# Kernel tuning notes

Hardware: AMD Instinct MI355X
Metric: run time of the kernel (lower is better)

Reference implementation:

```python
import jax, jax.numpy as jnp
import numpy as np

N_NODES = 50000
N_EDGES = 800000
NEG_SLOPE = 0.2


def _gat_layer(x, src, dst, W, al, ar, n_nodes):
    """Single multi-head GAT conv (DGL-style). Returns [N, H, D]."""
    H, D = al.shape
    feat = (x @ W).reshape(n_nodes, H, D)              # [N,H,D]
    el = jnp.einsum('nhd,hd->nh', feat, al)            # [N,H]
    er = jnp.einsum('nhd,hd->nh', feat, ar)            # [N,H]
    e = jax.nn.leaky_relu(el[src] + er[dst], NEG_SLOPE)  # [E,H]
    # numerically-stable edge softmax over incoming edges per dst node
    emax = jax.ops.segment_max(e, dst, num_segments=n_nodes)  # [N,H]
    emax = jnp.where(jnp.isfinite(emax), emax, 0.0)
    ee = jnp.exp(e - emax[dst])                        # [E,H]
    denom = jax.ops.segment_sum(ee, dst, num_segments=n_nodes)  # [N,H]
    alpha = ee / (denom[dst] + 1e-9)                   # [E,H]
    msg = alpha[:, :, None] * feat[src]                # [E,H,D]
    return jax.ops.segment_sum(msg, dst, num_segments=n_nodes)  # [N,H,D]


def setup_inputs() -> dict:
    key = jax.random.key(0)
    ks = jax.random.split(key, 9)
    features = jax.random.normal(ks[0], (N_NODES, 512), jnp.float32)
    src = jax.random.randint(ks[1], (N_EDGES,), 0, N_NODES)
    dst = jax.random.randint(ks[2], (N_EDGES,), 0, N_NODES)
    W1 = jax.random.normal(ks[3], (512, 256), jnp.float32) * 0.05
    al1 = jax.random.normal(ks[4], (8, 32), jnp.float32) * 0.05
    ar1 = jax.random.normal(ks[5], (8, 32), jnp.float32) * 0.05
    W2 = jax.random.normal(ks[6], (256, 320), jnp.float32) * 0.05
    al2 = jax.random.normal(ks[7], (8, 40), jnp.float32) * 0.05
    ar2 = jax.random.normal(ks[8], (8, 40), jnp.float32) * 0.05
    return {"features": features, "src": src, "dst": dst,
            "W1": W1, "al1": al1, "ar1": ar1,
            "W2": W2, "al2": al2, "ar2": ar2}


def reference(features, src, dst, W1, al1, ar1, W2, al2, ar2):
    n = features.shape[0]
    h = _gat_layer(features, src, dst, W1, al1, ar1, n)   # [N,8,32]
    h = jax.nn.elu(h.reshape(n, -1))                      # flatten(1) + ELU -> [N,256]
    h = _gat_layer(h, src, dst, W2, al2, ar2, n)          # [N,8,40]
    return h.mean(axis=1)                                 # head mean -> [N,40]
```

## Files before the change

kernel.cpp:

```cpp
#include <hip/hip_runtime.h>
#include <math.h>

typedef float f32x4 __attribute__((ext_vector_type(4)));
typedef __bf16 bf16x2 __attribute__((ext_vector_type(2)));
typedef __bf16 bf16x4 __attribute__((ext_vector_type(4)));
typedef __bf16 bf16x8 __attribute__((ext_vector_type(8)));


__global__ void hist_kernel(const int* __restrict__ dst, int* __restrict__ cnt, int E) {
    int e = blockIdx.x * blockDim.x + threadIdx.x;
    if (e < E) atomicAdd(&cnt[dst[e]], 1);
}

__global__ __launch_bounds__(256) void scan_blk(const int* __restrict__ cnt,
                                                int* __restrict__ incl,
                                                int* __restrict__ bsum, int n) {
    __shared__ int sd[256];
    const int t = threadIdx.x;
    int i = blockIdx.x * 256 + t;
    int v = (i < n) ? cnt[i] : 0;
    sd[t] = v;
    __syncthreads();
#pragma unroll
    for (int off = 1; off < 256; off <<= 1) {
        int x = (t >= off) ? sd[t - off] : 0;
        __syncthreads();
        sd[t] += x;
        __syncthreads();
    }
    if (i < n) incl[i] = sd[t];
    if (t == 255) bsum[blockIdx.x] = sd[255];
}

__global__ __launch_bounds__(256) void scan_top(const int* __restrict__ bsum,
                                                int* __restrict__ boff, int nb) {
    __shared__ int sd[256];
    const int t = threadIdx.x;
    int v = (t < nb) ? bsum[t] : 0;
    sd[t] = v;
    __syncthreads();
#pragma unroll
    for (int off = 1; off < 256; off <<= 1) {
        int x = (t >= off) ? sd[t - off] : 0;
        __syncthreads();
        sd[t] += x;
        __syncthreads();
    }
    if (t < nb) boff[t] = sd[t] - v;
}

__global__ void scan_fix(const int* __restrict__ incl, const int* __restrict__ boff,
                         const int* __restrict__ cnt, int* __restrict__ row_ptr,
                         int* __restrict__ cursor, int n) {
    int i = blockIdx.x * blockDim.x + threadIdx.x;
    if (i >= n) return;
    int total = incl[i] + boff[i >> 8];
    row_ptr[i + 1] = total;
    cursor[i] = total - cnt[i];
    if (i == 0) row_ptr[0] = 0;
}

__global__ void fill_kernel(const int* __restrict__ src, const int* __restrict__ dst,
                            int* __restrict__ cursor, int* __restrict__ ssrc,
                            int* __restrict__ sdst, int E) {
    int e = blockIdx.x * blockDim.x + threadIdx.x;
    if (e < E) {
        int d = dst[e];
        int pos = atomicAdd(&cursor[d], 1);
        ssrc[pos] = src[e];
        sdst[pos] = d;
    }
}

__global__ void split_w_kernel(const float* __restrict__ W, __bf16* __restrict__ Wth,
                               __bf16* __restrict__ Wtl, int K, int N) {
    int idx = blockIdx.x * blockDim.x + threadIdx.x;
    if (idx >= K * N) return;
    int k = idx / N, n = idx % N;
    float x = W[idx];
    __bf16 h = (__bf16)x;
    __bf16 l = (__bf16)(x - (float)h);
    Wth[(size_t)n * K + k] = h;
    Wtl[(size_t)n * K + k] = l;
}

template <int BN, int NREP>
__global__ __launch_bounds__(256, 2) void gemm_fused(
    const float* __restrict__ A, const __bf16* __restrict__ Bth,
    const __bf16* __restrict__ Btl, const float* __restrict__ al,
    const float* __restrict__ ar, __bf16* __restrict__ featb,
    float* __restrict__ el, float* __restrict__ er, int M, int K) {
    constexpr int WN = NREP * 16;
    constexpr int D = BN / 8;
    constexpr int HBN = BN / 2;

    struct Stage {
        __bf16 Ah[64][32];
        __bf16 Al[64][32];
        __bf16 Bh[BN][32];
        __bf16 Bl[BN][32];
    };
    union Smem {
        Stage s;
        float ctile[64][HBN + 4];
    };
    __shared__ __align__(16) Smem u;

    const int t = threadIdx.x;
    const int lane = t & 63;
    const int wid = t >> 6;
    const int row0 = blockIdx.x * 64;
    const int colw = wid * WN;
    const int fr = lane & 15;
    const int kg = (lane >> 4) * 8;

    f32x4 acc[4][NREP] = {};

    for (int k0 = 0; k0 < K; k0 += 32) {
#pragma unroll
        for (int p = 0; p < 2; ++p) {
            int idx = t + p * 256;
            int r = idx >> 3;
            int c4 = (idx & 7) * 4;
            int gr = row0 + r;
            if (gr >= M) gr = M - 1;
            float4 v = *(const float4*)&A[(size_t)gr * K + k0 + c4];
            __bf16 h0 = (__bf16)v.x, h1 = (__bf16)v.y, h2 = (__bf16)v.z, h3 = (__bf16)v.w;
            bf16x4 hv = {h0, h1, h2, h3};
            bf16x4 lv = {(__bf16)(v.x - (float)h0), (__bf16)(v.y - (float)h1),
                         (__bf16)(v.z - (float)h2), (__bf16)(v.w - (float)h3)};
            *(bf16x4*)&u.s.Ah[r][c4] = hv;
            *(bf16x4*)&u.s.Al[r][c4] = lv;
        }
#pragma unroll
        for (int p = 0; p < BN / 64; ++p) {
            int idx = t + p * 256;
            int n = idx >> 2;
            int c = (idx & 3) * 8;
            *(bf16x8*)&u.s.Bh[n][c] = *(const bf16x8*)&Bth[(size_t)n * K + k0 + c];
            *(bf16x8*)&u.s.Bl[n][c] = *(const bf16x8*)&Btl[(size_t)n * K + k0 + c];
        }
        __syncthreads();

        bf16x8 ah[4], alv[4], bh[NREP], bl[NREP];
#pragma unroll
        for (int m = 0; m < 4; ++m) {
            ah[m] = *(const bf16x8*)&u.s.Ah[fr + m * 16][kg];
            alv[m] = *(const bf16x8*)&u.s.Al[fr + m * 16][kg];
        }
#pragma unroll
        for (int n = 0; n < NREP; ++n) {
            bh[n] = *(const bf16x8*)&u.s.Bh[colw + n * 16 + fr][kg];
            bl[n] = *(const bf16x8*)&u.s.Bl[colw + n * 16 + fr][kg];
        }
#pragma unroll
        for (int m = 0; m < 4; ++m)
#pragma unroll
            for (int n = 0; n < NREP; ++n) {
                acc[m][n] = __builtin_amdgcn_mfma_f32_16x16x32_bf16(ah[m], bh[n], acc[m][n], 0, 0, 0);
                acc[m][n] = __builtin_amdgcn_mfma_f32_16x16x32_bf16(alv[m], bh[n], acc[m][n], 0, 0, 0);
                acc[m][n] = __builtin_amdgcn_mfma_f32_16x16x32_bf16(ah[m], bl[n], acc[m][n], 0, 0, 0);
            }
        __syncthreads();
    }

#pragma unroll
    for (int m = 0; m < 4; ++m) {
        int rbase = row0 + m * 16 + (lane >> 4) * 4;
#pragma unroll
        for (int n = 0; n < NREP; ++n) {
            int col = colw + n * 16 + fr;
#pragma unroll
            for (int i = 0; i < 4; ++i) {
                int r = rbase + i;
                if (r < M) featb[(size_t)r * BN + col] = (__bf16)acc[m][n][i];
            }
        }
    }

#pragma unroll
    for (int half = 0; half < 2; ++half) {
        __syncthreads();
        if ((wid >> 1) == half) {
            int cbase = colw - half * HBN;
#pragma unroll
            for (int m = 0; m < 4; ++m) {
                int rb = m * 16 + (lane >> 4) * 4;
#pragma unroll
                for (int n = 0; n < NREP; ++n) {
                    int lc = cbase + n * 16 + fr;
#pragma unroll
                    for (int i = 0; i < 4; ++i) u.ctile[rb + i][lc] = acc[m][n][i];
                }
            }
        }
        __syncthreads();
        int r = t & 63;
        int hh = t >> 6;
        int h = half * 4 + hh;
        float sl = 0.f, sr = 0.f;
#pragma unroll
        for (int d = 0; d < D; ++d) {
            float v = u.ctile[r][hh * D + d];
            sl += v * al[h * D + d];
            sr += v * ar[h * D + d];
        }
        int gr = row0 + r;
        if (gr < M) {
            el[(size_t)gr * 8 + h] = sl;
            er[(size_t)gr * 8 + h] = sr;
        }
    }
}

__device__ __forceinline__ float leaky02(float x) { return x > 0.f ? x : 0.2f * x; }

__global__ void edge_score_kernel(const int* __restrict__ ssrc, const int* __restrict__ sdst,
                                  const float* __restrict__ el, const float* __restrict__ er,
                                  float* __restrict__ pe, int E) {
    int pos = blockIdx.x * blockDim.x + threadIdx.x;
    if (pos >= E) return;
    int s = ssrc[pos], d = sdst[pos];
    float4 l0 = *(const float4*)&el[(size_t)s * 8];
    float4 l1 = *(const float4*)&el[(size_t)s * 8 + 4];
    float4 r0 = *(const float4*)&er[(size_t)d * 8];
    float4 r1 = *(const float4*)&er[(size_t)d * 8 + 4];
    float4 o0 = {leaky02(l0.x + r0.x), leaky02(l0.y + r0.y),
                 leaky02(l0.z + r0.z), leaky02(l0.w + r0.w)};
    float4 o1 = {leaky02(l1.x + r1.x), leaky02(l1.y + r1.y),
                 leaky02(l1.z + r1.z), leaky02(l1.w + r1.w)};
    *(float4*)&pe[(size_t)pos * 8] = o0;
    *(float4*)&pe[(size_t)pos * 8 + 4] = o1;
}

template <int D, int MODE>
__global__ __launch_bounds__(256) void gat_aggregate(
    const __bf16* __restrict__ featb, const float* __restrict__ pe,
    const int* __restrict__ row_ptr, const int* __restrict__ ssrc,
    float* __restrict__ out, int N) {
    constexpr int HD = 8 * D;
    constexpr int TAIL = HD - 256;
    __shared__ float red[4][MODE ? HD : 1];

    const int wid = threadIdx.x >> 6;
    const int lane = threadIdx.x & 63;
    const int n = blockIdx.x * 4 + wid;
    if (n >= N) return;

    const int beg = row_ptr[n];
    const int end = row_ptr[n + 1];
    const int hl = lane & 7;
    const int sl = lane >> 3;

    float m_l = -INFINITY;
    for (int idx = beg + sl; idx < end; idx += 8)
        m_l = fmaxf(m_l, pe[(size_t)idx * 8 + hl]);
    m_l = fmaxf(m_l, __shfl_xor(m_l, 8));
    m_l = fmaxf(m_l, __shfl_xor(m_l, 16));
    m_l = fmaxf(m_l, __shfl_xor(m_l, 32));
    float s_l = 0.f;
    for (int idx = beg + sl; idx < end; idx += 8)
        s_l += __expf(pe[(size_t)idx * 8 + hl] - m_l);
    s_l += __shfl_xor(s_l, 8);
    s_l += __shfl_xor(s_l, 16);
    s_l += __shfl_xor(s_l, 32);
    const float si_l = 1.0f / (s_l + 1e-9f);

    int hg[2], ht = 0;
#pragma unroll
    for (int g = 0; g < 2; ++g) hg[g] = (128 * g + 2 * lane) / D;
    if (TAIL) ht = (256 + lane) / D;

    float acc[2][2] = {};
    float acct = 0.f;
    int idx = beg;
    for (; idx + 4 <= end; idx += 4) {
        int ss[4];
        float aa[4];
#pragma unroll
        for (int uu = 0; uu < 4; ++uu) ss[uu] = ssrc[idx + uu];
#pragma unroll
        for (int uu = 0; uu < 4; ++uu)
            aa[uu] = __expf(pe[(size_t)(idx + uu) * 8 + hl] - m_l) * si_l;
        bf16x2 p[4][2];
        __bf16 pt[4];
#pragma unroll
        for (int uu = 0; uu < 4; ++uu) {
            const __bf16* f = featb + (size_t)ss[uu] * HD;
            p[uu][0] = *(const bf16x2*)&f[2 * lane];
            p[uu][1] = *(const bf16x2*)&f[128 + 2 * lane];
            if (TAIL) pt[uu] = f[256 + lane];
        }
#pragma unroll
        for (int uu = 0; uu < 4; ++uu) {
            float w0 = __shfl(aa[uu], hg[0]);
            float w1 = __shfl(aa[uu], hg[1]);
            acc[0][0] += w0 * (float)p[uu][0].x;
            acc[0][1] += w0 * (float)p[uu][0].y;
            acc[1][0] += w1 * (float)p[uu][1].x;
            acc[1][1] += w1 * (float)p[uu][1].y;
            if (TAIL) {
                float wt = __shfl(aa[uu], ht);
                acct += wt * (float)pt[uu];
            }
        }
    }
    for (; idx < end; ++idx) {
        int s = ssrc[idx];
        float a = __expf(pe[(size_t)idx * 8 + hl] - m_l) * si_l;
        const __bf16* f = featb + (size_t)s * HD;
        float w0 = __shfl(a, hg[0]);
        float w1 = __shfl(a, hg[1]);
        bf16x2 p0 = *(const bf16x2*)&f[2 * lane];
        bf16x2 p1 = *(const bf16x2*)&f[128 + 2 * lane];
        acc[0][0] += w0 * (float)p0.x;
        acc[0][1] += w0 * (float)p0.y;
        acc[1][0] += w1 * (float)p1.x;
        acc[1][1] += w1 * (float)p1.y;
        if (TAIL) {
            float wt = __shfl(a, ht);
            acct += wt * (float)f[256 + lane];
        }
    }

    if (MODE == 0) {
#pragma unroll
        for (int g = 0; g < 2; ++g) {
            float x0 = acc[g][0], x1 = acc[g][1];
            x0 = x0 > 0.f ? x0 : expm1f(x0);
            x1 = x1 > 0.f ? x1 : expm1f(x1);
            float2 v = {x0, x1};
            *(float2*)&out[(size_t)n * 256 + 128 * g + 2 * lane] = v;
        }
    } else {
#pragma unroll
        for (int g = 0; g < 2; ++g) {
            red[wid][128 * g + 2 * lane] = acc[g][0];
            red[wid][128 * g + 2 * lane + 1] = acc[g][1];
        }
        red[wid][256 + lane] = acct;
        if (lane < D) {
            float s = 0.f;
#pragma unroll
            for (int hh = 0; hh < 8; ++hh) s += red[wid][hh * D + lane];
            out[(size_t)n * D + lane] = s * 0.125f;
        }
    }
}


extern "C" void kernel_launch(void* const* d_in, const int* in_sizes, int n_in,
                              void* d_out, int out_size, void* d_ws, size_t ws_size,
                              hipStream_t stream) {
    const float* features = (const float*)d_in[0];
    const int* src = (const int*)d_in[1];
    const int* dst = (const int*)d_in[2];
    const float* W1 = (const float*)d_in[3];
    const float* al1 = (const float*)d_in[4];
    const float* ar1 = (const float*)d_in[5];
    const float* W2 = (const float*)d_in[6];
    const float* al2 = (const float*)d_in[7];
    const float* ar2 = (const float*)d_in[8];

    const int N = in_sizes[0] / 512;
    const int E = in_sizes[1];

    char* ws = (char*)d_ws;
    size_t off = 0;
    auto alloc = [&](size_t bytes) -> void* {
        void* p = ws + off;
        off = (off + bytes + 255) & ~(size_t)255;
        return p;
    };
    __bf16* feat1b = (__bf16*)alloc((size_t)N * 256 * 2);
    float* hbuf = (float*)alloc((size_t)N * 256 * 4);
    __bf16* feat2b = (__bf16*)alloc((size_t)N * 320 * 2);
    float* pe = (float*)alloc((size_t)E * 8 * 4);
    float* el1 = (float*)alloc((size_t)N * 8 * 4);
    float* er1 = (float*)alloc((size_t)N * 8 * 4);
    float* el2 = (float*)alloc((size_t)N * 8 * 4);
    float* er2 = (float*)alloc((size_t)N * 8 * 4);
    int* cnt = (int*)alloc((size_t)N * 4);
    int* incl = (int*)alloc((size_t)N * 4);
    int* row_ptr = (int*)alloc((size_t)(N + 1) * 4);
    int* cursor = (int*)alloc((size_t)N * 4);
    int* bsum = (int*)alloc(256 * 4);
    int* boff = (int*)alloc(256 * 4);
    int* ssrc = (int*)alloc((size_t)E * 4);
    int* sdst = (int*)alloc((size_t)E * 4);
    __bf16* Wt1h = (__bf16*)alloc((size_t)512 * 256 * 2);
    __bf16* Wt1l = (__bf16*)alloc((size_t)512 * 256 * 2);
    __bf16* Wt2h = (__bf16*)alloc((size_t)256 * 320 * 2);
    __bf16* Wt2l = (__bf16*)alloc((size_t)256 * 320 * 2);

    const int NB = (N + 255) / 256;

    hipMemsetAsync(cnt, 0, (size_t)N * 4, stream);
    hist_kernel<<<(E + 255) / 256, 256, 0, stream>>>(dst, cnt, E);
    scan_blk<<<NB, 256, 0, stream>>>(cnt, incl, bsum, N);
    scan_top<<<1, 256, 0, stream>>>(bsum, boff, NB);
    scan_fix<<<NB, 256, 0, stream>>>(incl, boff, cnt, row_ptr, cursor, N);
    fill_kernel<<<(E + 255) / 256, 256, 0, stream>>>(src, dst, cursor, ssrc, sdst, E);

    split_w_kernel<<<(512 * 256 + 255) / 256, 256, 0, stream>>>(W1, Wt1h, Wt1l, 512, 256);
    split_w_kernel<<<(256 * 320 + 255) / 256, 256, 0, stream>>>(W2, Wt2h, Wt2l, 256, 320);

    const int mblk = (N + 63) / 64;

    gemm_fused<256, 4><<<mblk, 256, 0, stream>>>(features, Wt1h, Wt1l, al1, ar1,
                                                 feat1b, el1, er1, N, 512);
    edge_score_kernel<<<(E + 255) / 256, 256, 0, stream>>>(ssrc, sdst, el1, er1, pe, E);
    gat_aggregate<32, 0>
        <<<(N + 3) / 4, 256, 0, stream>>>(feat1b, pe, row_ptr, ssrc, hbuf, N);

    gemm_fused<320, 5><<<mblk, 256, 0, stream>>>(hbuf, Wt2h, Wt2l, al2, ar2,
                                                 feat2b, el2, er2, N, 256);
    edge_score_kernel<<<(E + 255) / 256, 256, 0, stream>>>(ssrc, sdst, el2, er2, pe, E);
    gat_aggregate<40, 1>
        <<<(N + 3) / 4, 256, 0, stream>>>(feat2b, pe, row_ptr, ssrc, (float*)d_out, N);
}
```

Baseline: 387.9 us.

## Double-buffer A tiles in GEMM, read B from global, pre-split layer-2 input

The GEMM now double-buffers only the A tile in LDS, prefetching the next k-slice while the current one feeds MFMA. B fragments are loaded straight from global memory (L2-resident weights) instead of being staged in LDS. For the second layer, the aggregate kernel writes the ELU output already split into bf16 hi/lo halves, so the GEMM can use global_load_lds async copies instead of converting fp32 per tile. The el/er epilogue is restructured per wave to fit the smaller shared tile. The trade-off is more global traffic for B and a different epilogue synchronisation pattern.

```diff
diff --git a/kernel.cpp b/kernel.cpp
--- a/kernel.cpp
+++ b/kernel.cpp
@@ -84,25 +84,23 @@
     Wtl[(size_t)n * K + k] = l;
 }
 
-template <int BN, int NREP>
+template <int BN, int NREP, bool FP32A>
 __global__ __launch_bounds__(256, 2) void gemm_fused(
-    const float* __restrict__ A, const __bf16* __restrict__ Bth,
+    const float* __restrict__ Af, const __bf16* __restrict__ Ahg,
+    const __bf16* __restrict__ Alg, const __bf16* __restrict__ Bth,
     const __bf16* __restrict__ Btl, const float* __restrict__ al,
     const float* __restrict__ ar, __bf16* __restrict__ featb,
     float* __restrict__ el, float* __restrict__ er, int M, int K) {
     constexpr int WN = NREP * 16;
     constexpr int D = BN / 8;
-    constexpr int HBN = BN / 2;
-
-    struct Stage {
-        __bf16 Ah[64][32];
-        __bf16 Al[64][32];
-        __bf16 Bh[BN][32];
-        __bf16 Bl[BN][32];
+
+    struct StageT {
+        __bf16 Ah[2][64][32];
+        __bf16 Al[2][64][32];
     };
     union Smem {
-        Stage s;
-        float ctile[64][HBN + 4];
+        StageT s;
+        float ctile[64][WN + 1];
     };
     __shared__ __align__(16) Smem u;
 
@@ -114,44 +112,58 @@
     const int fr = lane & 15;
     const int kg = (lane >> 4) * 8;
 
-    f32x4 acc[4][NREP] = {};
-
-    for (int k0 = 0; k0 < K; k0 += 32) {
-#pragma unroll
-        for (int p = 0; p < 2; ++p) {
-            int idx = t + p * 256;
-            int r = idx >> 3;
-            int c4 = (idx & 7) * 4;
+    auto stageA = [&](int p, int k0) {
+        if constexpr (FP32A) {
+#pragma unroll
+            for (int pp = 0; pp < 2; ++pp) {
+                int idx = t + pp * 256;
+                int r = idx >> 3;
+                int c4 = (idx & 7) * 4;
+                int gr = row0 + r;
+                if (gr >= M) gr = M - 1;
+                float4 v = *(const float4*)&Af[(size_t)gr * K + k0 + c4];
+                __bf16 h0 = (__bf16)v.x, h1 = (__bf16)v.y, h2 = (__bf16)v.z,
+                       h3 = (__bf16)v.w;
+                bf16x4 hv = {h0, h1, h2, h3};
+                bf16x4 lv = {(__bf16)(v.x - (float)h0), (__bf16)(v.y - (float)h1),
+                             (__bf16)(v.z - (float)h2), (__bf16)(v.w - (float)h3)};
+                *(bf16x4*)&u.s.Ah[p][r][c4] = hv;
+                *(bf16x4*)&u.s.Al[p][r][c4] = lv;
+            }
+        } else {
+            int r = t >> 2;
+            int c = (t & 3) * 8;
             int gr = row0 + r;
             if (gr >= M) gr = M - 1;
-            float4 v = *(const float4*)&A[(size_t)gr * K + k0 + c4];
-            __bf16 h0 = (__bf16)v.x, h1 = (__bf16)v.y, h2 = (__bf16)v.z, h3 = (__bf16)v.w;
-            bf16x4 hv = {h0, h1, h2, h3};
-            bf16x4 lv = {(__bf16)(v.x - (float)h0), (__bf16)(v.y - (float)h1),
-                         (__bf16)(v.z - (float)h2), (__bf16)(v.w - (float)h3)};
-            *(bf16x4*)&u.s.Ah[r][c4] = hv;
-            *(bf16x4*)&u.s.Al[r][c4] = lv;
-        }
-#pragma unroll
-        for (int p = 0; p < BN / 64; ++p) {
-            int idx = t + p * 256;
-            int n = idx >> 2;
-            int c = (idx & 3) * 8;
-            *(bf16x8*)&u.s.Bh[n][c] = *(const bf16x8*)&Bth[(size_t)n * K + k0 + c];
-            *(bf16x8*)&u.s.Bl[n][c] = *(const bf16x8*)&Btl[(size_t)n * K + k0 + c];
-        }
-        __syncthreads();
-
-        bf16x8 ah[4], alv[4], bh[NREP], bl[NREP];
+            __builtin_amdgcn_global_load_lds(
+                (const __attribute__((address_space(1))) void*)&Ahg[(size_t)gr * K + k0 + c],
+                (__attribute__((address_space(3))) void*)&u.s.Ah[p][r][c], 16, 0, 0);
+            __builtin_amdgcn_global_load_lds(
+                (const __attribute__((address_space(1))) void*)&Alg[(size_t)gr * K + k0 + c],
+                (__attribute__((address_space(3))) void*)&u.s.Al[p][r][c], 16, 0, 0);
+        }
+    };
+
+    f32x4 acc[4][NREP] = {};
+
+    stageA(0, 0);
+    __syncthreads();
+
+    int p = 0;
+    for (int k0 = 0; k0 < K; k0 += 32) {
+        bf16x8 bh[NREP], bl[NREP];
+#pragma unroll
+        for (int n = 0; n < NREP; ++n) {
+            size_t boff = (size_t)(colw + n * 16 + fr) * K + k0 + kg;
+            bh[n] = *(const bf16x8*)&Bth[boff];
+            bl[n] = *(const bf16x8*)&Btl[boff];
+        }
+        if (k0 + 32 < K) stageA(p ^ 1, k0 + 32);
+        bf16x8 ah[4], alv[4];
 #pragma unroll
         for (int m = 0; m < 4; ++m) {
-            ah[m] = *(const bf16x8*)&u.s.Ah[fr + m * 16][kg];
-            alv[m] = *(const bf16x8*)&u.s.Al[fr + m * 16][kg];
-        }
-#pragma unroll
-        for (int n = 0; n < NREP; ++n) {
-            bh[n] = *(const bf16x8*)&u.s.Bh[colw + n * 16 + fr][kg];
-            bl[n] = *(const bf16x8*)&u.s.Bl[colw + n * 16 + fr][kg];
+            ah[m] = *(const bf16x8*)&u.s.Ah[p][fr + m * 16][kg];
+            alv[m] = *(const bf16x8*)&u.s.Al[p][fr + m * 16][kg];
         }
 #pragma unroll
         for (int m = 0; m < 4; ++m)
@@ -162,6 +174,7 @@
                 acc[m][n] = __builtin_amdgcn_mfma_f32_16x16x32_bf16(ah[m], bl[n], acc[m][n], 0, 0, 0);
             }
         __syncthreads();
+        p ^= 1;
     }
 
 #pragma unroll
@@ -179,36 +192,37 @@
     }
 
 #pragma unroll
-    for (int half = 0; half < 2; ++half) {
-        __syncthreads();
-        if ((wid >> 1) == half) {
-            int cbase = colw - half * HBN;
+    for (int q = 0; q < 4; ++q) {
+        __syncthreads();
+        if (wid == q) {
 #pragma unroll
             for (int m = 0; m < 4; ++m) {
                 int rb = m * 16 + (lane >> 4) * 4;
 #pragma unroll
                 for (int n = 0; n < NREP; ++n) {
-                    int lc = cbase + n * 16 + fr;
+                    int lc = n * 16 + fr;
 #pragma unroll
                     for (int i = 0; i < 4; ++i) u.ctile[rb + i][lc] = acc[m][n][i];
                 }
             }
         }
         __syncthreads();
-        int r = t & 63;
-        int hh = t >> 6;
-        int h = half * 4 + hh;
-        float sl = 0.f, sr = 0.f;
-#pragma unroll
-        for (int d = 0; d < D; ++d) {
-            float v = u.ctile[r][hh * D + d];
-            sl += v * al[h * D + d];
-            sr += v * ar[h * D + d];
-        }
-        int gr = row0 + r;
-        if (gr < M) {
-            el[(size_t)gr * 8 + h] = sl;
-            er[(size_t)gr * 8 + h] = sr;
+        if (t < 128) {
+            int r = t & 63;
+            int hh = t >> 6;
+            int h = q * 2 + hh;
+            float sl = 0.f, sr = 0.f;
+#pragma unroll
+            for (int d = 0; d < D; ++d) {
+                float v = u.ctile[r][hh * D + d];
+                sl += v * al[h * D + d];
+                sr += v * ar[h * D + d];
+            }
+            int gr = row0 + r;
+            if (gr < M) {
+                el[(size_t)gr * 8 + h] = sl;
+                er[(size_t)gr * 8 + h] = sr;
+            }
         }
     }
 }
@@ -237,7 +251,8 @@
 __global__ __launch_bounds__(256) void gat_aggregate(
     const __bf16* __restrict__ featb, const float* __restrict__ pe,
     const int* __restrict__ row_ptr, const int* __restrict__ ssrc,
-    float* __restrict__ out, int N) {
+    __bf16* __restrict__ outh, __bf16* __restrict__ outl,
+    float* __restrict__ outf, int N) {
     constexpr int HD = 8 * D;
     constexpr int TAIL = HD - 256;
     __shared__ float red[4][MODE ? HD : 1];
@@ -329,8 +344,11 @@
             float x0 = acc[g][0], x1 = acc[g][1];
             x0 = x0 > 0.f ? x0 : expm1f(x0);
             x1 = x1 > 0.f ? x1 : expm1f(x1);
-            float2 v = {x0, x1};
-            *(float2*)&out[(size_t)n * 256 + 128 * g + 2 * lane] = v;
+            __bf16 h0 = (__bf16)x0, h1 = (__bf16)x1;
+            bf16x2 vh = {h0, h1};
+            bf16x2 vl = {(__bf16)(x0 - (float)h0), (__bf16)(x1 - (float)h1)};
+            *(bf16x2*)&outh[(size_t)n * 256 + 128 * g + 2 * lane] = vh;
+            *(bf16x2*)&outl[(size_t)n * 256 + 128 * g + 2 * lane] = vl;
         }
     } else {
 #pragma unroll
@@ -343,7 +361,7 @@
             float s = 0.f;
 #pragma unroll
             for (int hh = 0; hh < 8; ++hh) s += red[wid][hh * D + lane];
-            out[(size_t)n * D + lane] = s * 0.125f;
+            outf[(size_t)n * D + lane] = s * 0.125f;
         }
     }
 }
@@ -373,7 +391,8 @@
         return p;
     };
     __bf16* feat1b = (__bf16*)alloc((size_t)N * 256 * 2);
-    float* hbuf = (float*)alloc((size_t)N * 256 * 4);
+    __bf16* h_hi = (__bf16*)alloc((size_t)N * 256 * 2);
+    __bf16* h_lo = (__bf16*)alloc((size_t)N * 256 * 2);
     __bf16* feat2b = (__bf16*)alloc((size_t)N * 320 * 2);
     float* pe = (float*)alloc((size_t)E * 8 * 4);
     float* el1 = (float*)alloc((size_t)N * 8 * 4);
@@ -407,15 +426,15 @@
 
     const int mblk = (N + 63) / 64;
 
-    gemm_fused<256, 4><<<mblk, 256, 0, stream>>>(features, Wt1h, Wt1l, al1, ar1,
-                                                 feat1b, el1, er1, N, 512);
+    gemm_fused<256, 4, true><<<mblk, 256, 0, stream>>>(
+        features, nullptr, nullptr, Wt1h, Wt1l, al1, ar1, feat1b, el1, er1, N, 512);
     edge_score_kernel<<<(E + 255) / 256, 256, 0, stream>>>(ssrc, sdst, el1, er1, pe, E);
-    gat_aggregate<32, 0>
-        <<<(N + 3) / 4, 256, 0, stream>>>(feat1b, pe, row_ptr, ssrc, hbuf, N);
-
-    gemm_fused<320, 5><<<mblk, 256, 0, stream>>>(hbuf, Wt2h, Wt2l, al2, ar2,
-                                                 feat2b, el2, er2, N, 256);
+    gat_aggregate<32, 0><<<(N + 3) / 4, 256, 0, stream>>>(
+        feat1b, pe, row_ptr, ssrc, h_hi, h_lo, nullptr, N);
+
+    gemm_fused<320, 5, false><<<mblk, 256, 0, stream>>>(
+        nullptr, h_hi, h_lo, Wt2h, Wt2l, al2, ar2, feat2b, el2, er2, N, 256);
     edge_score_kernel<<<(E + 255) / 256, 256, 0, stream>>>(ssrc, sdst, el2, er2, pe, E);
-    gat_aggregate<40, 1>
-        <<<(N + 3) / 4, 256, 0, stream>>>(feat2b, pe, row_ptr, ssrc, (float*)d_out, N);
-}
+    gat_aggregate<40, 1><<<(N + 3) / 4, 256, 0, stream>>>(
+        feat2b, pe, row_ptr, ssrc, nullptr, nullptr, (float*)d_out, N);
+}
```

Result: slower. 412.7 us (+6.4%).
